# Kernel optimization log

Measured on AMD Instinct MI355X. Metric: run time of the kernel, lower is better.

Reference implementation:

```python
import jax, jax.numpy as jnp
import numpy as np

EPS = 1e-5
B, N = 32, 2048


def fps(xyz, npoint):
    # farthest point sampling: xyz (B,N,3) -> int32 indices (B,npoint)
    b, n, _ = xyz.shape
    def step(carry, _):
        dist, last = carry
        p = jnp.take_along_axis(xyz, last[:, None, None], axis=1)  # (B,1,3)
        d = jnp.sum((xyz - p) ** 2, axis=-1)                       # (B,N)
        dist = jnp.minimum(dist, d)
        nxt = jnp.argmax(dist, axis=-1).astype(jnp.int32)
        return (dist, nxt), nxt
    init = (jnp.full((b, n), 1e10, xyz.dtype), jnp.zeros((b,), jnp.int32))
    _, rest = jax.lax.scan(step, init, None, length=npoint - 1)
    return jnp.concatenate([jnp.zeros((b, 1), jnp.int32), rest.T], axis=1)


def ball_query(radius, nsample, xyz, new_xyz):
    # replicates CUDA ball_query: first nsample in-radius indices, pad with first hit (0 if none)
    n = xyz.shape[1]
    d2 = jnp.sum((new_xyz[:, :, None, :] - xyz[:, None, :, :]) ** 2, axis=-1)  # (B,S,N)
    key = jnp.where(d2 < radius * radius, jnp.arange(n, dtype=jnp.int32), jnp.int32(n))
    srt = jnp.sort(key, axis=-1)[..., :nsample]                                # (B,S,K)
    first = srt[..., :1]
    first = jnp.where(first == n, 0, first)
    return jnp.where(srt == n, first, srt)


def gather_points(x, idx):
    # x (B,N,C), idx (B,...) int -> (B,...,C)
    b = x.shape[0]
    flat = idx.reshape(b, -1)
    out = jnp.take_along_axis(x, flat[..., None], axis=1)
    return out.reshape(idx.shape + (x.shape[-1],))


def mlp_maxpool(feat, weights, gammas, betas):
    # feat (B,C,S,K); shared 1x1 Conv2d + BatchNorm2d(train stats) + ReLU per layer, then max over K
    for W, g, bb in zip(weights, gammas, betas):
        y = jnp.einsum('bcsk,oc->bosk', feat, W)
        m = jnp.mean(y, axis=(0, 2, 3), keepdims=True)
        v = jnp.var(y, axis=(0, 2, 3), keepdims=True)
        feat = jax.nn.relu((y - m) / jnp.sqrt(v + EPS) * g[None, :, None, None] + bb[None, :, None, None])
    return jnp.max(feat, axis=-1)  # (B,C,S)


def setup_inputs() -> dict:
    key = jax.random.key(0)
    ks = jax.random.split(key, 8)
    pointcloud = jax.random.uniform(ks[0], (B, 3, N), jnp.float32, minval=-1.0, maxval=1.0)
    def w(k, o, i):
        return jax.random.normal(k, (o, i), jnp.float32) * (1.0 / np.sqrt(i))
    inp = {'pointcloud': pointcloud,
           'w1a': w(ks[1], 64, 6),   'g1a': jnp.ones((64,)),  'b1a': jnp.zeros((64,)),
           'w1b': w(ks[2], 128, 64), 'g1b': jnp.ones((128,)), 'b1b': jnp.zeros((128,)),
           'w2a': w(ks[3], 128, 134),'g2a': jnp.ones((128,)), 'b2a': jnp.zeros((128,)),
           'w2b': w(ks[4], 512, 128),'g2b': jnp.ones((512,)), 'b2b': jnp.zeros((512,)),
           'w3':  w(ks[5], 512, 515),'g3':  jnp.ones((512,)), 'b3':  jnp.zeros((512,))}
    return inp


def reference(pointcloud, w1a, g1a, b1a, w1b, g1b, b1b, w2a, g2a, b2a, w2b, g2b, b2b, w3, g3, b3):
    xyz = jnp.transpose(pointcloud, (0, 2, 1))  # (B,N,3)
    # --- SA1: fps 512, radius 0.23, nsample 48, mlp 6->64->128 ---
    fi1 = fps(xyz, 512)
    xyz1 = gather_points(xyz, fi1)                    # (B,512,3)
    ni1 = ball_query(0.23, 48, xyz, xyz1)             # (B,512,48)
    gx1 = gather_points(xyz, ni1)                     # (B,512,48,3)
    rel1 = gx1 - xyz1[:, :, None, :]
    f = jnp.concatenate([rel1, gx1], axis=-1).transpose(0, 3, 1, 2)  # (B,6,512,48)
    f1 = mlp_maxpool(f, [w1a, w1b], [g1a, g1b], [b1a, b1b])          # (B,128,512)
    # --- SA2: fps 128, radius 0.32, nsample 64, mlp 134->128->512 ---
    fi2 = fps(xyz1, 128)
    xyz2 = gather_points(xyz1, fi2)                   # (B,128,3)
    ni2 = ball_query(0.32, 64, xyz1, xyz2)            # (B,128,64)
    gx2 = gather_points(xyz1, ni2)                    # (B,128,64,3)
    rel2 = gx2 - xyz2[:, :, None, :]
    gf2 = gather_points(jnp.transpose(f1, (0, 2, 1)), ni2)           # (B,128,64,128)
    f = jnp.concatenate([rel2, gx2, gf2], axis=-1).transpose(0, 3, 1, 2)  # (B,134,128,64)
    f2 = mlp_maxpool(f, [w2a, w2b], [g2a, g2b], [b2a, b2b])          # (B,512,128)
    # --- SA3: group-all over 128 points, mlp 515->512 ---
    f = jnp.concatenate([xyz2, jnp.transpose(f2, (0, 2, 1))], axis=-1)    # (B,128,515)
    f = jnp.transpose(f, (0, 2, 1))[:, :, None, :]                        # (B,515,1,128)
    f3 = mlp_maxpool(f, [w3], [g3], [b3])                                 # (B,512,1)
    return f3[..., 0]                                                     # (B,512)
```

## Files before the change

kernel.cpp:

```cpp
#include <hip/hip_runtime.h>
#include <math.h>

constexpr int Bb = 32, Nn = 2048;
constexpr int S1 = 512, K1 = 48;
constexpr int S2 = 128, K2 = 64;

#define DEVI __device__ __forceinline__

DEVI float sq3(float dx, float dy, float dz) {
    return __fadd_rn(__fadd_rn(__fmul_rn(dx, dx), __fmul_rn(dy, dy)), __fmul_rn(dz, dz));
}

__global__ void k_transpose(const float* __restrict__ pc, float* __restrict__ xyz) {
    int i = blockIdx.x * blockDim.x + threadIdx.x;
    if (i >= Bb * Nn) return;
    int b = i / Nn;
    const float* s = pc + (size_t)b * 3 * Nn + (i % Nn);
    float* d = xyz + (size_t)i * 3;
    d[0] = s[0];
    d[1] = s[Nn];
    d[2] = s[2 * Nn];
}

__global__ void k_wtrans(const float* __restrict__ w2a, const float* __restrict__ w2b,
                         float* __restrict__ w2aT, float* __restrict__ w2bT) {
    int i = blockIdx.x * blockDim.x + threadIdx.x;
    if (i < 134 * 128) {
        int c = i >> 7, o = i & 127;
        w2aT[i] = w2a[(size_t)o * 134 + c];
    }
    if (i < 128 * 512) {
        int c = i >> 9, o = i & 511;
        w2bT[i] = w2b[(size_t)o * 128 + c];
    }
}

template <int PTS>
__global__ __launch_bounds__(256)
void k_fps_fast(const float* __restrict__ pts, int npoint, float* __restrict__ sel) {
    constexpr int N = PTS * 256;
    __shared__ float px[N], py[N], pz[N];
    __shared__ float rv[4];
    __shared__ int ri[4];
    int b = blockIdx.x, t = threadIdx.x;
    const float* base = pts + (size_t)b * N * 3;
    float dist[PTS];
    #pragma unroll
    for (int i = 0; i < PTS; ++i) {
        int j = i * 256 + t;
        px[j] = base[j * 3 + 0];
        py[j] = base[j * 3 + 1];
        pz[j] = base[j * 3 + 2];
        dist[i] = 1e10f;
    }
    if (t == 0) {
        float* o = sel + (size_t)b * npoint * 3;
        o[0] = base[0]; o[1] = base[1]; o[2] = base[2];
    }
    __syncthreads();
    float lx = px[0], ly = py[0], lz = pz[0];
    for (int it = 1; it < npoint; ++it) {
        float bv = -1.0f;
        int bi = 0;
        #pragma unroll
        for (int i = 0; i < PTS; ++i) {
            int j = i * 256 + t;
            float d = sq3(px[j] - lx, py[j] - ly, pz[j] - lz);
            float dd = fminf(dist[i], d);
            dist[i] = dd;
            if (dd > bv) { bv = dd; bi = j; }
        }
        #pragma unroll
        for (int off = 32; off > 0; off >>= 1) {
            float ov = __shfl_down(bv, off);
            int oi = __shfl_down(bi, off);
            if (ov > bv || (ov == bv && oi < bi)) { bv = ov; bi = oi; }
        }
        __syncthreads();
        if ((t & 63) == 0) { rv[t >> 6] = bv; ri[t >> 6] = bi; }
        __syncthreads();
        float v0 = rv[0];
        int i0 = ri[0];
        #pragma unroll
        for (int w = 1; w < 4; ++w) {
            float vw = rv[w]; int iw = ri[w];
            if (vw > v0 || (vw == v0 && iw < i0)) { v0 = vw; i0 = iw; }
        }
        lx = px[i0]; ly = py[i0]; lz = pz[i0];
        if (t == 0) {
            float* o = sel + ((size_t)b * npoint + it) * 3;
            o[0] = lx; o[1] = ly; o[2] = lz;
        }
    }
}

__global__ void k_ballquery_w(const float* __restrict__ src, const float* __restrict__ ctr,
                              int n, int m, int nsample, float r2, int* __restrict__ out) {
    int wid = blockIdx.x * (blockDim.x >> 6) + (threadIdx.x >> 6);
    int lane = threadIdx.x & 63;
    if (wid >= Bb * m) return;
    int b = wid / m;
    const float* sb = src + (size_t)b * n * 3;
    float cx = ctr[(size_t)wid * 3 + 0];
    float cy = ctr[(size_t)wid * 3 + 1];
    float cz = ctr[(size_t)wid * 3 + 2];
    int* ob = out + (size_t)wid * nsample;
    int cnt = 0, first = 0;
    for (int j0 = 0; j0 < n && cnt < nsample; j0 += 64) {
        int j = j0 + lane;
        float d2 = sq3(sb[j * 3 + 0] - cx, sb[j * 3 + 1] - cy, sb[j * 3 + 2] - cz);
        bool hit = d2 < r2;
        unsigned long long mask = __ballot(hit);
        if (cnt == 0 && mask) first = j0 + __ffsll(mask) - 1;
        int pos = cnt + __popcll(mask & ((1ull << lane) - 1ull));
        if (hit && pos < nsample) ob[pos] = j;
        cnt += __popcll(mask);
    }
    if (cnt < nsample)
        for (int k = cnt + lane; k < nsample; k += 64) ob[k] = first;
}

__global__ void k_zero_stats(double* dsum, double* dsq, int O) {
    int i = blockIdx.x * blockDim.x + threadIdx.x;
    if (i < O) { dsum[i] = 0.0; dsq[i] = 0.0; }
}

__global__ void k_finalize(const double* __restrict__ dsum, const double* __restrict__ dsq,
                           const float* __restrict__ g, float* __restrict__ mean,
                           float* __restrict__ scale, int O, double inv_count) {
    int o = blockIdx.x * blockDim.x + threadIdx.x;
    if (o < O) {
        double m = dsum[o] * inv_count;
        double v = dsq[o] * inv_count - m * m;
        mean[o] = (float)m;
        scale[o] = (float)((double)g[o] / sqrt(v + 1e-5));
    }
}

__global__ void k_applyMM(const float* __restrict__ gmx, const float* __restrict__ gmn,
                          const float* __restrict__ m, const float* __restrict__ s,
                          const float* __restrict__ beta, float* __restrict__ f,
                          long long total, int O) {
    long long i = (long long)blockIdx.x * blockDim.x + threadIdx.x;
    if (i >= total) return;
    int o = (int)(i % O);
    float sc = s[o];
    float pick = (sc >= 0.f) ? gmx[i] : gmn[i];
    f[i] = fmaxf((pick - m[o]) * sc + beta[o], 0.f);
}

__global__ __launch_bounds__(256)
void k_s1_statsA(const float* __restrict__ xyz, const float* __restrict__ xyz1,
                 const int* __restrict__ ni1, const float* __restrict__ w1a,
                 double* __restrict__ dsum, double* __restrict__ dsq) {
    __shared__ float red[256], red2[256];
    int t = threadIdx.x;
    float ls = 0.f, lsq = 0.f;
    for (int bs = blockIdx.x; bs < Bb * S1; bs += gridDim.x) {
        int b = bs >> 9;
        float cx = xyz1[bs * 3 + 0], cy = xyz1[bs * 3 + 1], cz = xyz1[bs * 3 + 2];
        for (int idx = t; idx < K1 * 64; idx += 256) {
            int k = idx >> 6, c = idx & 63;
            int j = ni1[bs * K1 + k];
            const float* g = xyz + ((size_t)b * Nn + j) * 3;
            float gx = g[0], gy = g[1], gz = g[2];
            const float* w = w1a + c * 6;
            float y = (gx - cx) * w[0] + (gy - cy) * w[1] + (gz - cz) * w[2]
                    + gx * w[3] + gy * w[4] + gz * w[5];
            ls += y; lsq += y * y;
        }
    }
    red[t] = ls; red2[t] = lsq;
    __syncthreads();
    if (t < 64) {
        double S = (double)red[t] + red[t + 64] + red[t + 128] + red[t + 192];
        double Q = (double)red2[t] + red2[t + 64] + red2[t + 128] + red2[t + 192];
        atomicAdd(&dsum[t], S); atomicAdd(&dsq[t], Q);
    }
}

constexpr int LDK1 = 50;
__global__ __launch_bounds__(256)
void k_s1_main(const float* __restrict__ xyz, const float* __restrict__ xyz1,
               const int* __restrict__ ni1, const float* __restrict__ w1a,
               const float* __restrict__ m1a, const float* __restrict__ s1a,
               const float* __restrict__ beta1a, const float* __restrict__ w1b,
               double* __restrict__ dsum, double* __restrict__ dsq,
               float* __restrict__ gmx, float* __restrict__ gmn) {
    __shared__ float x1T[64 * LDK1];
    __shared__ float wT[64 * 128];
    int t = threadIdx.x;
    int og = t >> 3, kg = t & 7;
    int o0 = og * 4, k0 = kg * 6;
    for (int idx = t; idx < 64 * 128; idx += 256)
        wT[idx] = w1b[(size_t)(idx & 127) * 64 + (idx >> 7)];
    __syncthreads();
    float lsB[4] = {0.f, 0.f, 0.f, 0.f}, lqB[4] = {0.f, 0.f, 0.f, 0.f};
    for (int bs = blockIdx.x; bs < Bb * S1; bs += gridDim.x) {
        int b = bs >> 9;
        float cx = xyz1[bs * 3 + 0], cy = xyz1[bs * 3 + 1], cz = xyz1[bs * 3 + 2];
        #pragma unroll
        for (int i = 0; i < 12; ++i) {
            int idx = t + i * 256;
            int k = idx >> 6, c = idx & 63;
            int j = ni1[bs * K1 + k];
            const float* g = xyz + ((size_t)b * Nn + j) * 3;
            float gx = g[0], gy = g[1], gz = g[2];
            const float* w = w1a + c * 6;
            float y = (gx - cx) * w[0] + (gy - cy) * w[1] + (gz - cz) * w[2]
                    + gx * w[3] + gy * w[4] + gz * w[5];
            x1T[c * LDK1 + k] = fmaxf((y - m1a[c]) * s1a[c] + beta1a[c], 0.f);
        }
        __syncthreads();
        float acc[24];
        #pragma unroll
        for (int i = 0; i < 24; ++i) acc[i] = 0.f;
        for (int c = 0; c < 64; ++c) {
            float4 wv = *(const float4*)&wT[c * 128 + o0];
            float2 xa = *(const float2*)&x1T[c * LDK1 + k0];
            float2 xb = *(const float2*)&x1T[c * LDK1 + k0 + 2];
            float2 xc = *(const float2*)&x1T[c * LDK1 + k0 + 4];
            float xs[6] = {xa.x, xa.y, xb.x, xb.y, xc.x, xc.y};
            float ws[4] = {wv.x, wv.y, wv.z, wv.w};
            #pragma unroll
            for (int i = 0; i < 4; ++i)
                #pragma unroll
                for (int j = 0; j < 6; ++j)
                    acc[i * 6 + j] = fmaf(ws[i], xs[j], acc[i * 6 + j]);
        }
        float mx[4], mn[4];
        #pragma unroll
        for (int i = 0; i < 4; ++i) {
            mx[i] = -1e30f; mn[i] = 1e30f;
            #pragma unroll
            for (int j = 0; j < 6; ++j) {
                float y = acc[i * 6 + j];
                lsB[i] += y; lqB[i] += y * y;
                mx[i] = fmaxf(mx[i], y); mn[i] = fminf(mn[i], y);
            }
        }
        #pragma unroll
        for (int off = 4; off > 0; off >>= 1)
            #pragma unroll
            for (int i = 0; i < 4; ++i) {
                mx[i] = fmaxf(mx[i], __shfl_down(mx[i], off));
                mn[i] = fminf(mn[i], __shfl_down(mn[i], off));
            }
        if (kg == 0) {
            *(float4*)&gmx[(size_t)bs * 128 + o0] = make_float4(mx[0], mx[1], mx[2], mx[3]);
            *(float4*)&gmn[(size_t)bs * 128 + o0] = make_float4(mn[0], mn[1], mn[2], mn[3]);
        }
        __syncthreads();
    }
    #pragma unroll
    for (int off = 4; off > 0; off >>= 1)
        #pragma unroll
        for (int i = 0; i < 4; ++i) {
            lsB[i] += __shfl_down(lsB[i], off);
            lqB[i] += __shfl_down(lqB[i], off);
        }
    if (kg == 0)
        #pragma unroll
        for (int i = 0; i < 4; ++i) {
            atomicAdd(&dsum[o0 + i], (double)lsB[i]);
            atomicAdd(&dsq[o0 + i], (double)lqB[i]);
        }
}

constexpr int LDK2 = 68;

DEVI void s2_gatherT(int t, int bs, const float* xyz1, const float* xyz2,
                     const int* ni2, const float* f1, float* xT) {
    int b = bs >> 7;
    float cx = xyz2[bs * 3 + 0], cy = xyz2[bs * 3 + 1], cz = xyz2[bs * 3 + 2];
    for (int idx = t; idx < K2 * 134; idx += 512) {
        int k = idx / 134, c = idx - k * 134;
        int j = ni2[bs * K2 + k];
        const float* p1 = xyz1 + ((size_t)b * S1 + j) * 3;
        float v;
        if (c < 3)      v = p1[c] - (c == 0 ? cx : (c == 1 ? cy : cz));
        else if (c < 6) v = p1[c - 3];
        else            v = f1[((size_t)b * S1 + j) * 128 + (c - 6)];
        xT[c * LDK2 + k] = v;
    }
}

__global__ __launch_bounds__(512, 4)
void k_s2_statsA(const float* __restrict__ xyz1, const float* __restrict__ xyz2,
                 const int* __restrict__ ni2, const float* __restrict__ f1,
                 const float* __restrict__ w2aT,
                 double* __restrict__ dsum, double* __restrict__ dsq) {
    __shared__ float xT[134 * LDK2];
    int t = threadIdx.x;
    int og = t >> 4, kg = t & 15;
    int o0 = og * 4, k0 = kg * 4;
    float ls[4] = {0.f, 0.f, 0.f, 0.f}, lq[4] = {0.f, 0.f, 0.f, 0.f};
    for (int bs = blockIdx.x; bs < Bb * S2; bs += gridDim.x) {
        __syncthreads();
        s2_gatherT(t, bs, xyz1, xyz2, ni2, f1, xT);
        __syncthreads();
        float acc[16];
        #pragma unroll
        for (int i = 0; i < 16; ++i) acc[i] = 0.f;
        for (int c = 0; c < 134; ++c) {
            float4 wv = *(const float4*)&w2aT[c * 128 + o0];
            float4 xv = *(const float4*)&xT[c * LDK2 + k0];
            float ws[4] = {wv.x, wv.y, wv.z, wv.w};
            float xs[4] = {xv.x, xv.y, xv.z, xv.w};
            #pragma unroll
            for (int i = 0; i < 4; ++i)
                #pragma unroll
                for (int j = 0; j < 4; ++j)
                    acc[i * 4 + j] = fmaf(ws[i], xs[j], acc[i * 4 + j]);
        }
        #pragma unroll
        for (int i = 0; i < 4; ++i)
            #pragma unroll
            for (int j = 0; j < 4; ++j) {
                float y = acc[i * 4 + j];
                ls[i] += y; lq[i] += y * y;
            }
    }
    #pragma unroll
    for (int off = 8; off > 0; off >>= 1)
        #pragma unroll
        for (int i = 0; i < 4; ++i) {
            ls[i] += __shfl_down(ls[i], off);
            lq[i] += __shfl_down(lq[i], off);
        }
    if (kg == 0)
        #pragma unroll
        for (int i = 0; i < 4; ++i) {
            atomicAdd(&dsum[o0 + i], (double)ls[i]);
            atomicAdd(&dsq[o0 + i], (double)lq[i]);
        }
}

__global__ __launch_bounds__(512, 4)
void k_s2_main(const float* __restrict__ xyz1, const float* __restrict__ xyz2,
               const int* __restrict__ ni2, const float* __restrict__ f1,
               const float* __restrict__ w2aT,
               const float* __restrict__ m2a, const float* __restrict__ s2a,
               const float* __restrict__ beta2a, const float* __restrict__ w2bT,
               double* __restrict__ dsum, double* __restrict__ dsq,
               float* __restrict__ gmx, float* __restrict__ gmn) {
    __shared__ float xT[134 * LDK2];
    __shared__ float x2T[128 * LDK2];
    int t = threadIdx.x;
    int ogA = t >> 4, kgA = t & 15;
    int o0A = ogA * 4, k0A = kgA * 4;
    int ogB = t >> 2, kgB = t & 3;
    int o0B = ogB * 4, k0B = kgB * 16;
    float lsB[4] = {0.f, 0.f, 0.f, 0.f}, lqB[4] = {0.f, 0.f, 0.f, 0.f};
    for (int bs = blockIdx.x; bs < Bb * S2; bs += gridDim.x) {
        __syncthreads();
        s2_gatherT(t, bs, xyz1, xyz2, ni2, f1, xT);
        __syncthreads();
        float acc[16];
        #pragma unroll
        for (int i = 0; i < 16; ++i) acc[i] = 0.f;
        for (int c = 0; c < 134; ++c) {
            float4 wv = *(const float4*)&w2aT[c * 128 + o0A];
            float4 xv = *(const float4*)&xT[c * LDK2 + k0A];
            float ws[4] = {wv.x, wv.y, wv.z, wv.w};
            float xs[4] = {xv.x, xv.y, xv.z, xv.w};
            #pragma unroll
            for (int i = 0; i < 4; ++i)
                #pragma unroll
                for (int j = 0; j < 4; ++j)
                    acc[i * 4 + j] = fmaf(ws[i], xs[j], acc[i * 4 + j]);
        }
        float4 mam = *(const float4*)&m2a[o0A];
        float4 sam = *(const float4*)&s2a[o0A];
        float4 bam = *(const float4*)&beta2a[o0A];
        float ma[4] = {mam.x, mam.y, mam.z, mam.w};
        float sa[4] = {sam.x, sam.y, sam.z, sam.w};
        float ba[4] = {bam.x, bam.y, bam.z, bam.w};
        #pragma unroll
        for (int i = 0; i < 4; ++i) {
            float4 v;
            v.x = fmaxf((acc[i * 4 + 0] - ma[i]) * sa[i] + ba[i], 0.f);
            v.y = fmaxf((acc[i * 4 + 1] - ma[i]) * sa[i] + ba[i], 0.f);
            v.z = fmaxf((acc[i * 4 + 2] - ma[i]) * sa[i] + ba[i], 0.f);
            v.w = fmaxf((acc[i * 4 + 3] - ma[i]) * sa[i] + ba[i], 0.f);
            *(float4*)&x2T[(o0A + i) * LDK2 + k0A] = v;
        }
        __syncthreads();
        float accB[64];
        #pragma unroll
        for (int i = 0; i < 64; ++i) accB[i] = 0.f;
        for (int c = 0; c < 128; ++c) {
            float4 wv = *(const float4*)&w2bT[c * 512 + o0B];
            const float* xr = &x2T[c * LDK2 + k0B];
            float4 x0 = *(const float4*)(xr);
            float4 x1 = *(const float4*)(xr + 4);
            float4 x2 = *(const float4*)(xr + 8);
            float4 x3 = *(const float4*)(xr + 12);
            float ws[4] = {wv.x, wv.y, wv.z, wv.w};
            float xs[16] = {x0.x, x0.y, x0.z, x0.w, x1.x, x1.y, x1.z, x1.w,
                            x2.x, x2.y, x2.z, x2.w, x3.x, x3.y, x3.z, x3.w};
            #pragma unroll
            for (int i = 0; i < 4; ++i)
                #pragma unroll
                for (int j = 0; j < 16; ++j)
                    accB[i * 16 + j] = fmaf(ws[i], xs[j], accB[i * 16 + j]);
        }
        float mxB[4], mnB[4];
        #pragma unroll
        for (int i = 0; i < 4; ++i) {
            mxB[i] = -1e30f; mnB[i] = 1e30f;
            #pragma unroll
            for (int j = 0; j < 16; ++j) {
                float y = accB[i * 16 + j];
                lsB[i] += y; lqB[i] += y * y;
                mxB[i] = fmaxf(mxB[i], y); mnB[i] = fminf(mnB[i], y);
            }
        }
        #pragma unroll
        for (int off = 2; off > 0; off >>= 1)
            #pragma unroll
            for (int i = 0; i < 4; ++i) {
                mxB[i] = fmaxf(mxB[i], __shfl_down(mxB[i], off));
                mnB[i] = fminf(mnB[i], __shfl_down(mnB[i], off));
            }
        if (kgB == 0) {
            *(float4*)&gmx[(size_t)bs * 512 + o0B] = make_float4(mxB[0], mxB[1], mxB[2], mxB[3]);
            *(float4*)&gmn[(size_t)bs * 512 + o0B] = make_float4(mnB[0], mnB[1], mnB[2], mnB[3]);
        }
    }
    #pragma unroll
    for (int off = 2; off > 0; off >>= 1)
        #pragma unroll
        for (int i = 0; i < 4; ++i) {
            lsB[i] += __shfl_down(lsB[i], off);
            lqB[i] += __shfl_down(lqB[i], off);
        }
    if (kgB == 0)
        #pragma unroll
        for (int i = 0; i < 4; ++i) {
            atomicAdd(&dsum[o0B + i], (double)lsB[i]);
            atomicAdd(&dsq[o0B + i], (double)lqB[i]);
        }
}

constexpr int X3_LD = 520;

__global__ __launch_bounds__(512)
void k_s3(const float* __restrict__ xyz2, const float* __restrict__ f2,
          const float* __restrict__ w3, double* __restrict__ dsum,
          double* __restrict__ dsq, float* __restrict__ gmx, float* __restrict__ gmn) {
    __shared__ float xt[16 * X3_LD];
    int b = blockIdx.x >> 3, kc = blockIdx.x & 7;
    int t = threadIdx.x;
    for (int idx = t; idx < 16 * X3_LD; idx += 512) {
        int rr = idx / X3_LD, c = idx - rr * X3_LD;
        int row = b * S2 + kc * 16 + rr;
        float v;
        if (c < 3)        v = xyz2[row * 3 + c];
        else if (c < 515) v = f2[(size_t)row * 512 + (c - 3)];
        else              v = 0.f;
        xt[idx] = v;
    }
    __syncthreads();
    float acc[16];
    #pragma unroll
    for (int rr = 0; rr < 16; ++rr) acc[rr] = 0.f;
    for (int ct = 0; ct < 16; ++ct) {
        float wr[32];
        #pragma unroll
        for (int i = 0; i < 32; ++i) wr[i] = w3[(size_t)t * 515 + ct * 32 + i];
        #pragma unroll
        for (int rr = 0; rr < 16; ++rr) {
            const float* xr = &xt[rr * X3_LD + ct * 32];
            #pragma unroll
            for (int j = 0; j < 8; ++j) {
                float4 x = *(const float4*)(xr + 4 * j);
                acc[rr] = fmaf(x.x, wr[4 * j + 0], acc[rr]);
                acc[rr] = fmaf(x.y, wr[4 * j + 1], acc[rr]);
                acc[rr] = fmaf(x.z, wr[4 * j + 2], acc[rr]);
                acc[rr] = fmaf(x.w, wr[4 * j + 3], acc[rr]);
            }
        }
    }
    {
        float wr[8];
        #pragma unroll
        for (int i = 0; i < 8; ++i) wr[i] = (i < 3) ? w3[(size_t)t * 515 + 512 + i] : 0.f;
        #pragma unroll
        for (int rr = 0; rr < 16; ++rr) {
            const float* xr = &xt[rr * X3_LD + 512];
            #pragma unroll
            for (int j = 0; j < 2; ++j) {
                float4 x = *(const float4*)(xr + 4 * j);
                acc[rr] = fmaf(x.x, wr[4 * j + 0], acc[rr]);
                acc[rr] = fmaf(x.y, wr[4 * j + 1], acc[rr]);
                acc[rr] = fmaf(x.z, wr[4 * j + 2], acc[rr]);
                acc[rr] = fmaf(x.w, wr[4 * j + 3], acc[rr]);
            }
        }
    }
    float ls = 0.f, lsq = 0.f, mxv = -1e30f, mnv = 1e30f;
    #pragma unroll
    for (int rr = 0; rr < 16; ++rr) {
        float y = acc[rr];
        ls += y; lsq += y * y;
        mxv = fmaxf(mxv, y); mnv = fminf(mnv, y);
    }
    atomicAdd(&dsum[t], (double)ls);
    atomicAdd(&dsq[t], (double)lsq);
    gmx[(size_t)blockIdx.x * 512 + t] = mxv;
    gmn[(size_t)blockIdx.x * 512 + t] = mnv;
}

__global__ void k_apply3(const float* __restrict__ gmx, const float* __restrict__ gmn,
                         const float* __restrict__ m, const float* __restrict__ s,
                         const float* __restrict__ beta, float* __restrict__ out) {
    int i = blockIdx.x * blockDim.x + threadIdx.x;
    if (i >= Bb * 512) return;
    int b = i >> 9, o = i & 511;
    float mx = -1e30f, mn = 1e30f;
    for (int ch = 0; ch < 8; ++ch) {
        mx = fmaxf(mx, gmx[(size_t)(b * 8 + ch) * 512 + o]);
        mn = fminf(mn, gmn[(size_t)(b * 8 + ch) * 512 + o]);
    }
    float sc = s[o];
    float pick = (sc >= 0.f) ? mx : mn;
    out[i] = fmaxf((pick - m[o]) * sc + beta[o], 0.f);
}

static inline size_t align256(size_t x) { return (x + 255) & ~(size_t)255; }

extern "C" void kernel_launch(void* const* d_in, const int* in_sizes, int n_in,
                              void* d_out, int out_size, void* d_ws, size_t ws_size,
                              hipStream_t stream) {
    const float* pc  = (const float*)d_in[0];
    const float* w1a = (const float*)d_in[1];
    const float* g1a = (const float*)d_in[2];
    const float* b1a = (const float*)d_in[3];
    const float* w1b = (const float*)d_in[4];
    const float* g1b = (const float*)d_in[5];
    const float* b1b = (const float*)d_in[6];
    const float* w2a = (const float*)d_in[7];
    const float* g2a = (const float*)d_in[8];
    const float* b2a = (const float*)d_in[9];
    const float* w2b = (const float*)d_in[10];
    const float* g2b = (const float*)d_in[11];
    const float* b2b = (const float*)d_in[12];
    const float* w3  = (const float*)d_in[13];
    const float* g3  = (const float*)d_in[14];
    const float* b3  = (const float*)d_in[15];
    float* out = (float*)d_out;

    char* ws = (char*)d_ws;
    size_t off = 0;
    auto alloc = [&](size_t bytes) { void* p = ws + off; off += align256(bytes); return p; };

    float* xyz   = (float*)alloc(sizeof(float) * Bb * Nn * 3);
    float* xyz1  = (float*)alloc(sizeof(float) * Bb * S1 * 3);
    float* xyz2  = (float*)alloc(sizeof(float) * Bb * S2 * 3);
    int*   ni1   = (int*)alloc(sizeof(int) * Bb * S1 * K1);
    int*   ni2   = (int*)alloc(sizeof(int) * Bb * S2 * K2);
    float* gmx1  = (float*)alloc(sizeof(float) * (size_t)Bb * S1 * 128);
    float* gmn1  = (float*)alloc(sizeof(float) * (size_t)Bb * S1 * 128);
    float* gmx2  = (float*)alloc(sizeof(float) * (size_t)Bb * S2 * 512);
    float* gmn2  = (float*)alloc(sizeof(float) * (size_t)Bb * S2 * 512);
    float* gmx3  = (float*)alloc(sizeof(float) * 256 * 512);
    float* gmn3  = (float*)alloc(sizeof(float) * 256 * 512);
    float* w2aT  = (float*)alloc(sizeof(float) * 134 * 128);
    float* w2bT  = (float*)alloc(sizeof(float) * 128 * 512);
    double* dsum = (double*)alloc(sizeof(double) * 512);
    double* dsq  = (double*)alloc(sizeof(double) * 512);
    float* m1a = (float*)alloc(sizeof(float) * 64);
    float* s1a = (float*)alloc(sizeof(float) * 64);
    float* m1b = (float*)alloc(sizeof(float) * 128);
    float* s1b = (float*)alloc(sizeof(float) * 128);
    float* m2a = (float*)alloc(sizeof(float) * 128);
    float* s2a = (float*)alloc(sizeof(float) * 128);
    float* m2b = (float*)alloc(sizeof(float) * 512);
    float* s2b = (float*)alloc(sizeof(float) * 512);
    float* m3  = (float*)alloc(sizeof(float) * 512);
    float* s3  = (float*)alloc(sizeof(float) * 512);
    float* f1 = gmx1;
    float* f2 = gmx2;

    k_transpose<<<(Bb * Nn + 255) / 256, 256, 0, stream>>>(pc, xyz);
    k_wtrans<<<256, 256, 0, stream>>>(w2a, w2b, w2aT, w2bT);
    k_fps_fast<8><<<Bb, 256, 0, stream>>>(xyz, S1, xyz1);
    k_ballquery_w<<<(Bb * S1) / 4, 256, 0, stream>>>(xyz, xyz1, Nn, S1, K1,
                                                     (float)(0.23 * 0.23), ni1);
    k_zero_stats<<<2, 256, 0, stream>>>(dsum, dsq, 512);
    k_s1_statsA<<<2048, 256, 0, stream>>>(xyz, xyz1, ni1, w1a, dsum, dsq);
    k_finalize<<<2, 256, 0, stream>>>(dsum, dsq, g1a, m1a, s1a, 64,
                                      1.0 / ((double)Bb * S1 * K1));
    k_zero_stats<<<2, 256, 0, stream>>>(dsum, dsq, 512);
    k_s1_main<<<1024, 256, 0, stream>>>(xyz, xyz1, ni1, w1a, m1a, s1a, b1a, w1b,
                                        dsum, dsq, gmx1, gmn1);
    k_finalize<<<2, 256, 0, stream>>>(dsum, dsq, g1b, m1b, s1b, 128,
                                      1.0 / ((double)Bb * S1 * K1));
    {
        long long tot = (long long)Bb * S1 * 128;
        k_applyMM<<<(int)((tot + 255) / 256), 256, 0, stream>>>(gmx1, gmn1, m1b, s1b, b1b,
                                                                f1, tot, 128);
    }
    k_fps_fast<2><<<Bb, 256, 0, stream>>>(xyz1, S2, xyz2);
    k_ballquery_w<<<(Bb * S2) / 4, 256, 0, stream>>>(xyz1, xyz2, S1, S2, K2,
                                                     (float)(0.32 * 0.32), ni2);
    k_zero_stats<<<2, 256, 0, stream>>>(dsum, dsq, 512);
    k_s2_statsA<<<1024, 512, 0, stream>>>(xyz1, xyz2, ni2, f1, w2aT, dsum, dsq);
    k_finalize<<<2, 256, 0, stream>>>(dsum, dsq, g2a, m2a, s2a, 128,
                                      1.0 / ((double)Bb * S2 * K2));
    k_zero_stats<<<2, 256, 0, stream>>>(dsum, dsq, 512);
    k_s2_main<<<1024, 512, 0, stream>>>(xyz1, xyz2, ni2, f1, w2aT, m2a, s2a, b2a, w2bT,
                                        dsum, dsq, gmx2, gmn2);
    k_finalize<<<2, 256, 0, stream>>>(dsum, dsq, g2b, m2b, s2b, 512,
                                      1.0 / ((double)Bb * S2 * K2));
    {
        long long tot = (long long)Bb * S2 * 512;
        k_applyMM<<<(int)((tot + 255) / 256), 256, 0, stream>>>(gmx2, gmn2, m2b, s2b, b2b,
                                                                f2, tot, 512);
    }
    k_zero_stats<<<2, 256, 0, stream>>>(dsum, dsq, 512);
    k_s3<<<256, 512, 0, stream>>>(xyz2, f2, w3, dsum, dsq, gmx3, gmn3);
    k_finalize<<<2, 256, 0, stream>>>(dsum, dsq, g3, m3, s3, 512,
                                      1.0 / ((double)Bb * S2));
    k_apply3<<<(Bb * 512 + 255) / 256, 256, 0, stream>>>(gmx3, gmn3, m3, s3, b3, out);
}
```

Before: 1.993 ms.

## Compute SA1 first-layer BN stats from input moments; process two centroids per block

The first-layer batch-norm statistics for SA1 are now derived from the 6-dim input's first and second moments (27 sums) plus a tiny finalize kernel that computes the mean and variance for each output channel through the weight matrix, instead of evaluating all 64 outputs per sample. k_s1_main now uses 512 threads handling two centroids per iteration with double-buffered shared tiles. The occupancy hint on k_s2_main is relaxed. The moment form computes variance as E[y^2]-mean^2, which risks cancellation, and the larger shared footprint may lower occupancy.

```diff
diff --git a/kernel.cpp b/kernel.cpp
--- a/kernel.cpp
+++ b/kernel.cpp
@@ -150,16 +150,97 @@
 }
 
 __global__ __launch_bounds__(256)
-void k_s1_statsA(const float* __restrict__ xyz, const float* __restrict__ xyz1,
-                 const int* __restrict__ ni1, const float* __restrict__ w1a,
-                 double* __restrict__ dsum, double* __restrict__ dsq) {
-    __shared__ float red[256], red2[256];
+void k_s1_moments(const float* __restrict__ xyz, const float* __restrict__ xyz1,
+                  const int* __restrict__ ni1, double* __restrict__ dG) {
+    __shared__ float wsum[4][27];
     int t = threadIdx.x;
-    float ls = 0.f, lsq = 0.f;
-    for (int bs = blockIdx.x; bs < Bb * S1; bs += gridDim.x) {
+    float p[27];
+    #pragma unroll
+    for (int v = 0; v < 27; ++v) p[v] = 0.f;
+    const int total = Bb * S1 * K1;
+    for (int i = blockIdx.x * 256 + t; i < total; i += gridDim.x * 256) {
+        int bs = i / K1;
+        int b = bs >> 9;
+        int j = ni1[i];
+        const float* g = xyz + ((size_t)b * Nn + j) * 3;
+        float cx = xyz1[bs * 3 + 0], cy = xyz1[bs * 3 + 1], cz = xyz1[bs * 3 + 2];
+        float f[6] = {g[0] - cx, g[1] - cy, g[2] - cz, g[0], g[1], g[2]};
+        int idx = 6;
+        #pragma unroll
+        for (int c = 0; c < 6; ++c) {
+            p[c] += f[c];
+            #pragma unroll
+            for (int d = c; d < 6; ++d) p[idx++] += f[c] * f[d];
+        }
+    }
+    #pragma unroll
+    for (int v = 0; v < 27; ++v)
+        #pragma unroll
+        for (int off = 32; off > 0; off >>= 1)
+            p[v] += __shfl_down(p[v], off);
+    if ((t & 63) == 0)
+        #pragma unroll
+        for (int v = 0; v < 27; ++v) wsum[t >> 6][v] = p[v];
+    __syncthreads();
+    if (t < 27) {
+        double s = (double)wsum[0][t] + wsum[1][t] + wsum[2][t] + wsum[3][t];
+        atomicAdd(&dG[t], s);
+    }
+}
+
+__global__ void k_fin1a(const double* __restrict__ dG, const float* __restrict__ w1a,
+                        const float* __restrict__ g1a, float* __restrict__ m1a,
+                        float* __restrict__ s1a, double inv_n) {
+    int o = threadIdx.x;
+    if (o >= 64) return;
+    double w[6];
+    #pragma unroll
+    for (int c = 0; c < 6; ++c) w[c] = (double)w1a[o * 6 + c];
+    double mean = 0.0;
+    #pragma unroll
+    for (int c = 0; c < 6; ++c) mean += w[c] * dG[c];
+    mean *= inv_n;
+    double ey2 = 0.0;
+    int idx = 6;
+    #pragma unroll
+    for (int c = 0; c < 6; ++c)
+        #pragma unroll
+        for (int d = c; d < 6; ++d, ++idx) {
+            double term = w[c] * w[d] * dG[idx];
+            ey2 += (d == c) ? term : 2.0 * term;
+        }
+    ey2 *= inv_n;
+    double var = ey2 - mean * mean;
+    m1a[o] = (float)mean;
+    s1a[o] = (float)((double)g1a[o] / sqrt(var + 1e-5));
+}
+
+constexpr int LDK1 = 50;
+__global__ __launch_bounds__(512)
+void k_s1_main(const float* __restrict__ xyz, const float* __restrict__ xyz1,
+               const int* __restrict__ ni1, const float* __restrict__ w1a,
+               const float* __restrict__ m1a, const float* __restrict__ s1a,
+               const float* __restrict__ beta1a, const float* __restrict__ w1b,
+               double* __restrict__ dsum, double* __restrict__ dsq,
+               float* __restrict__ gmx, float* __restrict__ gmn) {
+    __shared__ float x1T[2 * 64 * LDK1];
+    __shared__ float wT[64 * 128];
+    int t = threadIdx.x;
+    int half = t >> 8, tl = t & 255;
+    float* x1h = x1T + half * 64 * LDK1;
+    int og = tl >> 3, kg = tl & 7;
+    int o0 = og * 4, k0 = kg * 6;
+    for (int idx = t; idx < 64 * 128; idx += 512)
+        wT[idx] = w1b[(size_t)(idx & 127) * 64 + (idx >> 7)];
+    __syncthreads();
+    float lsB[4] = {0.f, 0.f, 0.f, 0.f}, lqB[4] = {0.f, 0.f, 0.f, 0.f};
+    for (int p = blockIdx.x; p < Bb * S1 / 2; p += gridDim.x) {
+        int bs = p * 2 + half;
         int b = bs >> 9;
         float cx = xyz1[bs * 3 + 0], cy = xyz1[bs * 3 + 1], cz = xyz1[bs * 3 + 2];
-        for (int idx = t; idx < K1 * 64; idx += 256) {
+        #pragma unroll
+        for (int i = 0; i < 12; ++i) {
+            int idx = tl + i * 256;
             int k = idx >> 6, c = idx & 63;
             int j = ni1[bs * K1 + k];
             const float* g = xyz + ((size_t)b * Nn + j) * 3;
@@ -167,49 +248,7 @@
             const float* w = w1a + c * 6;
             float y = (gx - cx) * w[0] + (gy - cy) * w[1] + (gz - cz) * w[2]
                     + gx * w[3] + gy * w[4] + gz * w[5];
-            ls += y; lsq += y * y;
-        }
-    }
-    red[t] = ls; red2[t] = lsq;
-    __syncthreads();
-    if (t < 64) {
-        double S = (double)red[t] + red[t + 64] + red[t + 128] + red[t + 192];
-        double Q = (double)red2[t] + red2[t + 64] + red2[t + 128] + red2[t + 192];
-        atomicAdd(&dsum[t], S); atomicAdd(&dsq[t], Q);
-    }
-}
-
-constexpr int LDK1 = 50;
-__global__ __launch_bounds__(256)
-void k_s1_main(const float* __restrict__ xyz, const float* __restrict__ xyz1,
-               const int* __restrict__ ni1, const float* __restrict__ w1a,
-               const float* __restrict__ m1a, const float* __restrict__ s1a,
-               const float* __restrict__ beta1a, const float* __restrict__ w1b,
-               double* __restrict__ dsum, double* __restrict__ dsq,
-               float* __restrict__ gmx, float* __restrict__ gmn) {
-    __shared__ float x1T[64 * LDK1];
-    __shared__ float wT[64 * 128];
-    int t = threadIdx.x;
-    int og = t >> 3, kg = t & 7;
-    int o0 = og * 4, k0 = kg * 6;
-    for (int idx = t; idx < 64 * 128; idx += 256)
-        wT[idx] = w1b[(size_t)(idx & 127) * 64 + (idx >> 7)];
-    __syncthreads();
-    float lsB[4] = {0.f, 0.f, 0.f, 0.f}, lqB[4] = {0.f, 0.f, 0.f, 0.f};
-    for (int bs = blockIdx.x; bs < Bb * S1; bs += gridDim.x) {
-        int b = bs >> 9;
-        float cx = xyz1[bs * 3 + 0], cy = xyz1[bs * 3 + 1], cz = xyz1[bs * 3 + 2];
-        #pragma unroll
-        for (int i = 0; i < 12; ++i) {
-            int idx = t + i * 256;
-            int k = idx >> 6, c = idx & 63;
-            int j = ni1[bs * K1 + k];
-            const float* g = xyz + ((size_t)b * Nn + j) * 3;
-            float gx = g[0], gy = g[1], gz = g[2];
-            const float* w = w1a + c * 6;
-            float y = (gx - cx) * w[0] + (gy - cy) * w[1] + (gz - cz) * w[2]
-                    + gx * w[3] + gy * w[4] + gz * w[5];
-            x1T[c * LDK1 + k] = fmaxf((y - m1a[c]) * s1a[c] + beta1a[c], 0.f);
+            x1h[c * LDK1 + k] = fmaxf((y - m1a[c]) * s1a[c] + beta1a[c], 0.f);
         }
         __syncthreads();
         float acc[24];
@@ -217,9 +256,9 @@
         for (int i = 0; i < 24; ++i) acc[i] = 0.f;
         for (int c = 0; c < 64; ++c) {
             float4 wv = *(const float4*)&wT[c * 128 + o0];
-            float2 xa = *(const float2*)&x1T[c * LDK1 + k0];
-            float2 xb = *(const float2*)&x1T[c * LDK1 + k0 + 2];
-            float2 xc = *(const float2*)&x1T[c * LDK1 + k0 + 4];
+            float2 xa = *(const float2*)&x1h[c * LDK1 + k0];
+            float2 xb = *(const float2*)&x1h[c * LDK1 + k0 + 2];
+            float2 xc = *(const float2*)&x1h[c * LDK1 + k0 + 4];
             float xs[6] = {xa.x, xa.y, xb.x, xb.y, xc.x, xc.y};
             float ws[4] = {wv.x, wv.y, wv.z, wv.w};
             #pragma unroll
@@ -336,7 +375,7 @@
         }
 }
 
-__global__ __launch_bounds__(512, 4)
+__global__ __launch_bounds__(512)
 void k_s2_main(const float* __restrict__ xyz1, const float* __restrict__ xyz2,
                const int* __restrict__ ni2, const float* __restrict__ f1,
                const float* __restrict__ w2aT,
@@ -589,11 +628,11 @@
     k_ballquery_w<<<(Bb * S1) / 4, 256, 0, stream>>>(xyz, xyz1, Nn, S1, K1,
                                                      (float)(0.23 * 0.23), ni1);
     k_zero_stats<<<2, 256, 0, stream>>>(dsum, dsq, 512);
-    k_s1_statsA<<<2048, 256, 0, stream>>>(xyz, xyz1, ni1, w1a, dsum, dsq);
-    k_finalize<<<2, 256, 0, stream>>>(dsum, dsq, g1a, m1a, s1a, 64,
-                                      1.0 / ((double)Bb * S1 * K1));
+    k_s1_moments<<<1024, 256, 0, stream>>>(xyz, xyz1, ni1, dsum);
+    k_fin1a<<<1, 64, 0, stream>>>(dsum, w1a, g1a, m1a, s1a,
+                                  1.0 / ((double)Bb * S1 * K1));
     k_zero_stats<<<2, 256, 0, stream>>>(dsum, dsq, 512);
-    k_s1_main<<<1024, 256, 0, stream>>>(xyz, xyz1, ni1, w1a, m1a, s1a, b1a, w1b,
+    k_s1_main<<<1024, 512, 0, stream>>>(xyz, xyz1, ni1, w1a, m1a, s1a, b1a, w1b,
                                         dsum, dsq, gmx1, gmn1);
     k_finalize<<<2, 256, 0, stream>>>(dsum, dsq, g1b, m1b, s1b, 128,
                                       1.0 / ((double)Bb * S1 * K1));
```

Measured after the change: 2.080 ms. 4.4% more time.
